# Performance work log

Hardware: AMD Instinct MI355X
Metric: run time of the kernel (lower is better)

## Reference

```python
import jax, jax.numpy as jnp
import numpy as np

K = 3          # kernel_size
STRIDE = 1
PAD = 1
DIL = 1


def setup_inputs() -> dict:
    key = jax.random.key(0)
    k1, k2, k3, k4, k5 = jax.random.split(key, 5)
    x = jax.random.normal(k1, (4, 64, 128, 128), jnp.float32)
    weight = jax.random.normal(k2, (64, 64, K, K), jnp.float32) * 0.05   # [O, C, K, K]
    bias = jax.random.normal(k3, (64,), jnp.float32) * 0.05
    # offset conv params: small nonzero so offsets actually exercise bilinear sampling
    offset_w = jax.random.normal(k4, (2 * K * K, 64, K, K), jnp.float32) * 0.01
    offset_b = jax.random.normal(k5, (2 * K * K,), jnp.float32) * 0.1
    return {"x": x, "weight": weight, "bias": bias,
            "offset_w": offset_w, "offset_b": offset_b}


def _conv2d(x, w, b):
    y = jax.lax.conv_general_dilated(
        x, w, window_strides=(STRIDE, STRIDE),
        padding=((PAD, PAD), (PAD, PAD)), rhs_dilation=(DIL, DIL),
        dimension_numbers=("NCHW", "OIHW", "NCHW"))
    return y + b[None, :, None, None]


def _bilinear_sample(img, ys, xs):
    # img: [C, H, W]; ys, xs: [KK, Ho, Wo] float sampling coords
    H, W = img.shape[1], img.shape[2]
    y0 = jnp.floor(ys)
    x0 = jnp.floor(xs)
    y1 = y0 + 1.0
    x1 = x0 + 1.0
    wy1 = ys - y0
    wx1 = xs - x0
    wy0 = 1.0 - wy1
    wx0 = 1.0 - wx1

    def gather(yy, xx):
        valid = (yy >= 0) & (yy <= H - 1) & (xx >= 0) & (xx <= W - 1)
        yi = jnp.clip(yy, 0, H - 1).astype(jnp.int32)
        xi = jnp.clip(xx, 0, W - 1).astype(jnp.int32)
        v = img[:, yi, xi]                     # [C, KK, Ho, Wo]
        return v * valid.astype(img.dtype)

    return (gather(y0, x0) * (wy0 * wx0) + gather(y0, x1) * (wy0 * wx1)
            + gather(y1, x0) * (wy1 * wx0) + gather(y1, x1) * (wy1 * wx1))


def reference(x, weight, bias, offset_w, offset_b):
    B, C, H, W = x.shape
    KK = K * K
    # offsets: [B, 2*K*K, Ho, Wo], per-location (dy, dx) for each kernel tap
    offset = _conv2d(x, offset_w, offset_b)
    Ho, Wo = offset.shape[2], offset.shape[3]
    off = offset.reshape(B, KK, 2, Ho, Wo)
    dy, dx = off[:, :, 0], off[:, :, 1]        # [B, KK, Ho, Wo]

    ki, kj = jnp.meshgrid(jnp.arange(K), jnp.arange(K), indexing="ij")
    ki = ki.reshape(KK).astype(x.dtype)
    kj = kj.reshape(KK).astype(x.dtype)
    oy = (jnp.arange(Ho) * STRIDE - PAD).astype(x.dtype)
    ox = (jnp.arange(Wo) * STRIDE - PAD).astype(x.dtype)
    base_y = oy[None, :, None] + (ki * DIL)[:, None, None]   # [KK, Ho, 1]
    base_x = ox[None, None, :] + (kj * DIL)[:, None, None]   # [KK, 1, Wo]
    ys = base_y[None] + dy                                   # [B, KK, Ho, Wo]
    xs = base_x[None] + dx

    # sampled: [B, C, KK, Ho, Wo]
    sampled = jax.vmap(_bilinear_sample)(x, ys, xs)
    w = weight.reshape(weight.shape[0], C, KK)
    out = jnp.einsum("bckhw,ock->bohw", sampled, w) + bias[None, :, None, None]
    return out
```

## Files before the change

kernel.cpp:

```cpp
#include <hip/hip_runtime.h>
#include <hip/hip_bf16.h>

#define B_ 4
#define C_ 64
#define H_ 128
#define W_ 128
#define HW_ (H_ * W_)
#define OCH_ 18

typedef __attribute__((ext_vector_type(2)))  _Float16 half2v;
typedef __attribute__((ext_vector_type(8)))  _Float16 half8;
typedef __attribute__((ext_vector_type(16))) float    f32x16;

#define W2B_ELEMS (9 * 2 * 4 * 64 * 8)
#define W2A_ELEMS (36 * 64 * 8)

#define PSTRIDE_B (6 * 128 * 16 + 16)
#define WIN_BYTES (8 * PSTRIDE_B)
#define OFFL_OFS  WIN_BYTES
#define OFFW_B    (OCH_ * 32 * 4)
#define SMEM_BYTES (WIN_BYTES + 8 * OFFW_B)

__device__ __forceinline__ unsigned short f2h(float f) {
  _Float16 h = (_Float16)f;
  return *reinterpret_cast<unsigned short*>(&h);
}
__device__ __forceinline__ half2v pkrtz(float a, float b) {
  auto p = __builtin_amdgcn_cvt_pkrtz(a, b);
  return *reinterpret_cast<half2v*>(&p);
}
__device__ __forceinline__ int swz256(int x) { return (x & 7) * 32 + (x >> 3); }
__device__ __forceinline__ int SWU(int row, int col) {
  return (((row << 7) + (col & ~3) + ((col & 3) ^ ((col >> 3) & 3))) << 4);
}

__global__ __launch_bounds__(256) void pack_w_only(
    const float* __restrict__ wmain, const float* __restrict__ offw,
    unsigned short* __restrict__ ws_u) {
  int idx = blockIdx.x * 256 + threadIdx.x;
  if (idx < W2B_ELEMS) {
    int i = idx & 7, lane = (idx >> 3) & 63, s = (idx >> 9) & 3;
    int mq = (idx >> 11) & 1, t = idx >> 12;
    int o = mq * 32 + (lane & 31);
    int c = 16 * s + (lane >> 5) * 8 + i;
    ws_u[idx] = f2h(wmain[(o * 64 + c) * 9 + t]);
  } else if (idx < W2B_ELEMS + W2A_ELEMS) {
    int j = idx - W2B_ELEMS;
    int i = j & 7, lane = (j >> 3) & 63, s = j >> 9;
    int kg = 16 * s + (lane >> 5) * 8 + i;
    int t = kg >> 6, c = kg & 63, oc = lane & 31;
    ws_u[idx] = (oc < OCH_) ? f2h(offw[(oc * 64 + c) * 9 + t]) : (unsigned short)0;
  }
}

template<int T>
__device__ __forceinline__ void tap_fast(
    const float* __restrict__ offl, int pxl, int ho, int ho0, int px,
    int lane, int laneh, const char* __restrict__ smem,
    const unsigned short* __restrict__ w2b,
    f32x16& acc0, f32x16& acc1, unsigned& fm) {
  constexpr int KI = T / 3, KJ = T - 3 * (T / 3);
  const float dy = offl[(2 * T) * 32 + pxl];
  const float dx = offl[(2 * T + 1) * 32 + pxl];
  const float ys = (float)(ho - 1 + KI) + dy;
  const float xs = (float)(px - 1 + KJ) + dx;
  const float y0f = floorf(ys), x0f = floorf(xs);
  const int y0 = (int)y0f, x0 = (int)x0f;
  const int y1 = y0 + 1, x1 = x0 + 1;
  const float wy1 = ys - y0f, wx1 = xs - x0f;
  const float wy0 = 1.f - wy1, wx0 = 1.f - wx1;
  const bool vy0 = (unsigned)y0 < (unsigned)H_, vy1 = (unsigned)y1 < (unsigned)H_;
  const bool vx0 = (unsigned)x0 < (unsigned)W_, vx1 = (unsigned)x1 < (unsigned)W_;
  const float g00 = (vy0 && vx0) ? wy0 * wx0 : 0.f;
  const float g01 = (vy0 && vx1) ? wy0 * wx1 : 0.f;
  const float g10 = (vy1 && vx0) ? wy1 * wx0 : 0.f;
  const float g11 = (vy1 && vx1) ? wy1 * wx1 : 0.f;
  const int yc0 = min(max(y0, 0), H_ - 1), yc1 = min(max(y1, 0), H_ - 1);
  const int xc0 = min(max(x0, 0), W_ - 1), xc1 = min(max(x1, 0), W_ - 1);
  const int rr0 = yc0 - ho0 + 2, rr1 = yc1 - ho0 + 2;
  const bool wr0 = (unsigned)rr0 < 6u, wr1 = (unsigned)rr1 < 6u;
  const float gg00 = wr0 ? g00 : 0.f, gg01 = wr0 ? g01 : 0.f;
  const float gg10 = wr1 ? g10 : 0.f, gg11 = wr1 ? g11 : 0.f;
  if (__any((!wr0 & (vy0 & (vx0 | vx1))) | (!wr1 & (vy1 & (vx0 | vx1)))))
    fm |= (1u << T);
  const int cr0 = min(max(rr0, 0), 5), cr1 = min(max(rr1, 0), 5);
  const int u00 = SWU(cr0, xc0), u01 = SWU(cr0, xc1);
  const int u10 = SWU(cr1, xc0), u11 = SWU(cr1, xc1);
  half2v G00; G00.x = G00.y = (_Float16)gg00;
  half2v G01; G01.x = G01.y = (_Float16)gg01;
  half2v G10; G10.x = G10.y = (_Float16)gg10;
  half2v G11; G11.x = G11.y = (_Float16)gg11;
  const unsigned short* wt2 = w2b + T * 4096;

  #pragma unroll
  for (int ss = 0; ss < 4; ++ss) {
    const char* pb = smem + (2 * ss + laneh) * PSTRIDE_B;
    const half8 c00 = *(const half8*)(pb + u00);
    const half8 c01 = *(const half8*)(pb + u01);
    const half8 c10 = *(const half8*)(pb + u10);
    const half8 c11 = *(const half8*)(pb + u11);
    const half2v* p00 = (const half2v*)&c00;
    const half2v* p01 = (const half2v*)&c01;
    const half2v* p10 = (const half2v*)&c10;
    const half2v* p11 = (const half2v*)&c11;
    union { half8 v; half2v h[4]; } bf;
    #pragma unroll
    for (int d = 0; d < 4; ++d)
      bf.h[d] = p00[d] * G00 + p01[d] * G01 + p10[d] * G10 + p11[d] * G11;
    const half8 a0 = *(const half8*)&wt2[(ss * 64 + lane) * 8];
    const half8 a1 = *(const half8*)&wt2[((4 + ss) * 64 + lane) * 8];
    acc0 = __builtin_amdgcn_mfma_f32_32x32x16_f16(a0, bf.v, acc0, 0, 0, 0);
    acc1 = __builtin_amdgcn_mfma_f32_32x32x16_f16(a1, bf.v, acc1, 0, 0, 0);
  }
}

__global__ __launch_bounds__(512, 2) void deform_fused9(
    const float* __restrict__ x, const float* __restrict__ bias,
    const float* __restrict__ ob, const unsigned short* __restrict__ w2b,
    const unsigned short* __restrict__ w2a, float* __restrict__ out) {
  const int blk = swz256(blockIdx.x);
  const int ho0 = (blk & 63) * 2;
  const int b   = blk >> 6;
  const int tid = threadIdx.x;
  const int lane = tid & 63;
  const int wave = tid >> 6;
  const int r_off = wave >> 2;
  const int pair  = wave & 3;
  const int ho = ho0 + r_off;
  const int pxl = lane & 31;
  const int px = pair * 32 + pxl;
  const int laneh = lane >> 5;

  __shared__ __align__(16) char smem[SMEM_BYTES];

  const float* xb = x + (size_t)b * C_ * HW_;
  #pragma unroll
  for (int it = 0; it < 3; ++it) {
    const int u = tid + it * 512;
    const int row  = u >> 8;
    const int p    = (u >> 5) & 7;
    const int col4 = u & 31;
    const int srow = min(H_ - 1, max(0, ho0 - 2 + row));
    const float* bp = xb + (size_t)(p * 8) * HW_ + srow * W_ + col4 * 4;
    float4 f[8];
    #pragma unroll
    for (int i = 0; i < 8; ++i) f[i] = *(const float4*)(bp + (size_t)i * HW_);
    char* outb = smem + p * PSTRIDE_B;
    #pragma unroll
    for (int j = 0; j < 4; ++j) {
      union { half8 v; half2v h[4]; } o;
      #pragma unroll
      for (int k = 0; k < 4; ++k)
        o.h[k] = pkrtz(reinterpret_cast<const float*>(&f[2 * k])[j],
                       reinterpret_cast<const float*>(&f[2 * k + 1])[j]);
      *(half8*)(outb + SWU(row, col4 * 4 + j)) = o.v;
    }
  }
  __syncthreads();

  f32x16 pacc_a, pacc_b;
  #pragma unroll
  for (int r = 0; r < 16; ++r) { pacc_a[r] = 0.f; pacc_b[r] = 0.f; }

  #pragma unroll 1
  for (int sq = 0; sq < 18; ++sq) {
    #pragma unroll
    for (int h = 0; h < 2; ++h) {
      const int s = 2 * sq + h;
      const int t = s >> 2;
      const int ki = (t >= 6) ? 2 : ((t >= 3) ? 1 : 0);
      const int kj = t - 3 * ki;
      const int row = ho - 1 + ki;
      const int col = px - 1 + kj;
      half8 bfr = {0, 0, 0, 0, 0, 0, 0, 0};
      if (((unsigned)row < (unsigned)H_) && ((unsigned)col < (unsigned)W_))
        bfr = *(const half8*)(smem + ((s & 3) * 2 + laneh) * PSTRIDE_B
                              + SWU(ki + 1 + r_off, col));
      const half8 afr = *(const half8*)&w2a[((size_t)s * 64 + lane) * 8];
      if (h)
        pacc_b = __builtin_amdgcn_mfma_f32_32x32x16_f16(afr, bfr, pacc_b, 0, 0, 0);
      else
        pacc_a = __builtin_amdgcn_mfma_f32_32x32x16_f16(afr, bfr, pacc_a, 0, 0, 0);
    }
  }

  float* offl = (float*)(smem + OFFL_OFS + wave * OFFW_B);
  #pragma unroll
  for (int reg = 0; reg < 16; ++reg) {
    const int oc = (reg & 3) + 8 * (reg >> 2) + 4 * laneh;
    if (oc < OCH_) offl[oc * 32 + pxl] = pacc_a[reg] + pacc_b[reg] + ob[oc];
  }

  f32x16 acc0, acc1;
  #pragma unroll
  for (int r = 0; r < 16; ++r) { acc0[r] = 0.f; acc1[r] = 0.f; }
  unsigned fm = 0;

  tap_fast<0>(offl, pxl, ho, ho0, px, lane, laneh, smem, w2b, acc0, acc1, fm);
  tap_fast<1>(offl, pxl, ho, ho0, px, lane, laneh, smem, w2b, acc0, acc1, fm);
  tap_fast<2>(offl, pxl, ho, ho0, px, lane, laneh, smem, w2b, acc0, acc1, fm);
  tap_fast<3>(offl, pxl, ho, ho0, px, lane, laneh, smem, w2b, acc0, acc1, fm);
  tap_fast<4>(offl, pxl, ho, ho0, px, lane, laneh, smem, w2b, acc0, acc1, fm);
  tap_fast<5>(offl, pxl, ho, ho0, px, lane, laneh, smem, w2b, acc0, acc1, fm);
  tap_fast<6>(offl, pxl, ho, ho0, px, lane, laneh, smem, w2b, acc0, acc1, fm);
  tap_fast<7>(offl, pxl, ho, ho0, px, lane, laneh, smem, w2b, acc0, acc1, fm);
  tap_fast<8>(offl, pxl, ho, ho0, px, lane, laneh, smem, w2b, acc0, acc1, fm);

  if (__builtin_expect(fm != 0, 0)) {
    #pragma unroll 1
    for (int t = 0; t < 9; ++t) {
      if (!((fm >> t) & 1)) continue;
      const int ki = (t >= 6) ? 2 : ((t >= 3) ? 1 : 0);
      const int kj = t - 3 * ki;
      const float dy = offl[(2 * t) * 32 + pxl];
      const float dx = offl[(2 * t + 1) * 32 + pxl];
      const float ys = (float)(ho - 1 + ki) + dy;
      const float xs = (float)(px - 1 + kj) + dx;
      const float y0f = floorf(ys), x0f = floorf(xs);
      const int y0 = (int)y0f, x0 = (int)x0f;
      const int y1 = y0 + 1, x1 = x0 + 1;
      const float wy1 = ys - y0f, wx1 = xs - x0f;
      const float wy0 = 1.f - wy1, wx0 = 1.f - wx1;
      const bool vy0 = (unsigned)y0 < (unsigned)H_, vy1 = (unsigned)y1 < (unsigned)H_;
      const bool vx0 = (unsigned)x0 < (unsigned)W_, vx1 = (unsigned)x1 < (unsigned)W_;
      float g00 = (vy0 && vx0) ? wy0 * wx0 : 0.f;
      float g01 = (vy0 && vx1) ? wy0 * wx1 : 0.f;
      float g10 = (vy1 && vx0) ? wy1 * wx0 : 0.f;
      float g11 = (vy1 && vx1) ? wy1 * wx1 : 0.f;
      const int yc0 = min(max(y0, 0), H_ - 1), yc1 = min(max(y1, 0), H_ - 1);
      const int xc0 = min(max(x0, 0), W_ - 1), xc1 = min(max(x1, 0), W_ - 1);
      const bool wr0 = (unsigned)(yc0 - ho0 + 2) < 6u;
      const bool wr1 = (unsigned)(yc1 - ho0 + 2) < 6u;
      g00 = wr0 ? 0.f : g00; g01 = wr0 ? 0.f : g01;
      g10 = wr1 ? 0.f : g10; g11 = wr1 ? 0.f : g11;
      const unsigned short* wt2 = w2b + t * 4096;
      #pragma unroll 1
      for (int ss = 0; ss < 4; ++ss) {
        union { half8 v; _Float16 e[8]; } bf;
        #pragma unroll
        for (int i = 0; i < 8; ++i) {
          const float* img = xb + (size_t)((2 * ss + laneh) * 8 + i) * HW_;
          float v = g00 * img[yc0 * W_ + xc0] + g01 * img[yc0 * W_ + xc1]
                  + g10 * img[yc1 * W_ + xc0] + g11 * img[yc1 * W_ + xc1];
          bf.e[i] = (_Float16)v;
        }
        const half8 a0 = *(const half8*)&wt2[(ss * 64 + lane) * 8];
        const half8 a1 = *(const half8*)&wt2[((4 + ss) * 64 + lane) * 8];
        acc0 = __builtin_amdgcn_mfma_f32_32x32x16_f16(a0, bf.v, acc0, 0, 0, 0);
        acc1 = __builtin_amdgcn_mfma_f32_32x32x16_f16(a1, bf.v, acc1, 0, 0, 0);
      }
    }
  }

  #pragma unroll
  for (int reg = 0; reg < 16; ++reg) {
    const int row = (reg & 3) + 8 * (reg >> 2) + 4 * laneh;
    out[((b * 64 + row)      * H_ + ho) * W_ + px] = acc0[reg] + bias[row];
    out[((b * 64 + 32 + row) * H_ + ho) * W_ + px] = acc1[reg] + bias[32 + row];
  }
}

extern "C" void kernel_launch(void* const* d_in, const int* in_sizes, int n_in,
                              void* d_out, int out_size, void* d_ws, size_t ws_size,
                              hipStream_t stream) {
  const float* x    = (const float*)d_in[0];
  const float* wt   = (const float*)d_in[1];
  const float* bias = (const float*)d_in[2];
  const float* ow   = (const float*)d_in[3];
  const float* ob   = (const float*)d_in[4];
  float* out = (float*)d_out;

  unsigned short* ws_u = (unsigned short*)d_ws;
  unsigned short* w2b  = ws_u;
  unsigned short* w2a  = ws_u + W2B_ELEMS;

  const int pack_blocks = (W2B_ELEMS + W2A_ELEMS + 255) / 256;
  pack_w_only<<<pack_blocks, 256, 0, stream>>>(wt, ow, ws_u);

  deform_fused9<<<B_ * (H_ / 2), 512, 0, stream>>>(x, bias, ob, w2b, w2a, out);
}
```

Before: 36.90 us.

## Split deform taps across wave groups per row with LDS reduction

Each block now handles a single output row instead of two. The two groups of four waves split the nine deformable taps between them (4 and 5) and combine partial accumulators through an LDS reduction. Offsets are pulled straight from the offset-conv MFMA registers with shuffles, so they no longer make a round trip through LDS. The smaller LDS window raises the launch-bounds occupancy hint, and the out-of-window fallback becomes a per-tap wave-uniform branch. The price is twice as many blocks, each loading its own 5-row halo, so input loads and the offset conv are duplicated, and there is an extra barrier plus reduction traffic.

```diff
diff --git a/kernel.cpp b/kernel.cpp
--- a/kernel.cpp
+++ b/kernel.cpp
@@ -15,11 +15,9 @@
 #define W2B_ELEMS (9 * 2 * 4 * 64 * 8)
 #define W2A_ELEMS (36 * 64 * 8)
 
-#define PSTRIDE_B (6 * 128 * 16 + 16)
+#define PSTRIDE_B (5 * 128 * 16)
 #define WIN_BYTES (8 * PSTRIDE_B)
-#define OFFL_OFS  WIN_BYTES
-#define OFFW_B    (OCH_ * 32 * 4)
-#define SMEM_BYTES (WIN_BYTES + 8 * OFFW_B)
+#define SMEM_BYTES WIN_BYTES
 
 __device__ __forceinline__ unsigned short f2h(float f) {
   _Float16 h = (_Float16)f;
@@ -29,7 +27,7 @@
   auto p = __builtin_amdgcn_cvt_pkrtz(a, b);
   return *reinterpret_cast<half2v*>(&p);
 }
-__device__ __forceinline__ int swz256(int x) { return (x & 7) * 32 + (x >> 3); }
+__device__ __forceinline__ int swz512(int x) { return (x & 7) * 64 + (x >> 3); }
 __device__ __forceinline__ int SWU(int row, int col) {
   return (((row << 7) + (col & ~3) + ((col & 3) ^ ((col >> 3) & 3))) << 4);
 }
@@ -54,14 +52,12 @@
 }
 
 template<int T>
-__device__ __forceinline__ void tap_fast(
-    const float* __restrict__ offl, int pxl, int ho, int ho0, int px,
-    int lane, int laneh, const char* __restrict__ smem,
+__device__ __forceinline__ void tap_full(
+    float dy, float dx, int ho, int px, int lane, int laneh,
+    const char* __restrict__ smem, const float* __restrict__ xb,
     const unsigned short* __restrict__ w2b,
-    f32x16& acc0, f32x16& acc1, unsigned& fm) {
+    f32x16& acc0, f32x16& acc1) {
   constexpr int KI = T / 3, KJ = T - 3 * (T / 3);
-  const float dy = offl[(2 * T) * 32 + pxl];
-  const float dx = offl[(2 * T + 1) * 32 + pxl];
   const float ys = (float)(ho - 1 + KI) + dy;
   const float xs = (float)(px - 1 + KJ) + dx;
   const float y0f = floorf(ys), x0f = floorf(xs);
@@ -77,32 +73,52 @@
   const float g11 = (vy1 && vx1) ? wy1 * wx1 : 0.f;
   const int yc0 = min(max(y0, 0), H_ - 1), yc1 = min(max(y1, 0), H_ - 1);
   const int xc0 = min(max(x0, 0), W_ - 1), xc1 = min(max(x1, 0), W_ - 1);
-  const int rr0 = yc0 - ho0 + 2, rr1 = yc1 - ho0 + 2;
-  const bool wr0 = (unsigned)rr0 < 6u, wr1 = (unsigned)rr1 < 6u;
-  const float gg00 = wr0 ? g00 : 0.f, gg01 = wr0 ? g01 : 0.f;
-  const float gg10 = wr1 ? g10 : 0.f, gg11 = wr1 ? g11 : 0.f;
-  if (__any((!wr0 & (vy0 & (vx0 | vx1))) | (!wr1 & (vy1 & (vx0 | vx1)))))
-    fm |= (1u << T);
-  const int cr0 = min(max(rr0, 0), 5), cr1 = min(max(rr1, 0), 5);
+  const int rr0 = yc0 - ho + 2, rr1 = yc1 - ho + 2;
+  const bool in = ((unsigned)rr0 < 5u) & ((unsigned)rr1 < 5u);
+  const unsigned short* wt2 = w2b + T * 4096;
+
+  if (__builtin_expect(__any(!in), 0)) {
+    #pragma unroll 1
+    for (int ss = 0; ss < 4; ++ss) {
+      union { half8 v; _Float16 e[8]; } bf;
+      #pragma unroll
+      for (int i = 0; i < 8; ++i) {
+        const float* img = xb + (size_t)((2 * ss + laneh) * 8 + i) * HW_;
+        float v = g00 * img[yc0 * W_ + xc0] + g01 * img[yc0 * W_ + xc1]
+                + g10 * img[yc1 * W_ + xc0] + g11 * img[yc1 * W_ + xc1];
+        bf.e[i] = (_Float16)v;
+      }
+      const half8 a0 = *(const half8*)&wt2[(ss * 64 + lane) * 8];
+      const half8 a1 = *(const half8*)&wt2[((4 + ss) * 64 + lane) * 8];
+      acc0 = __builtin_amdgcn_mfma_f32_32x32x16_f16(a0, bf.v, acc0, 0, 0, 0);
+      acc1 = __builtin_amdgcn_mfma_f32_32x32x16_f16(a1, bf.v, acc1, 0, 0, 0);
+    }
+    return;
+  }
+
+  const int cr0 = min(max(rr0, 0), 4), cr1 = min(max(rr1, 0), 4);
   const int u00 = SWU(cr0, xc0), u01 = SWU(cr0, xc1);
   const int u10 = SWU(cr1, xc0), u11 = SWU(cr1, xc1);
-  half2v G00; G00.x = G00.y = (_Float16)gg00;
-  half2v G01; G01.x = G01.y = (_Float16)gg01;
-  half2v G10; G10.x = G10.y = (_Float16)gg10;
-  half2v G11; G11.x = G11.y = (_Float16)gg11;
-  const unsigned short* wt2 = w2b + T * 4096;
-
+  half2v G00; G00.x = G00.y = (_Float16)g00;
+  half2v G01; G01.x = G01.y = (_Float16)g01;
+  half2v G10; G10.x = G10.y = (_Float16)g10;
+  half2v G11; G11.x = G11.y = (_Float16)g11;
+
+  half8 c00[4], c01[4], c10[4], c11[4];
   #pragma unroll
   for (int ss = 0; ss < 4; ++ss) {
     const char* pb = smem + (2 * ss + laneh) * PSTRIDE_B;
-    const half8 c00 = *(const half8*)(pb + u00);
-    const half8 c01 = *(const half8*)(pb + u01);
-    const half8 c10 = *(const half8*)(pb + u10);
-    const half8 c11 = *(const half8*)(pb + u11);
-    const half2v* p00 = (const half2v*)&c00;
-    const half2v* p01 = (const half2v*)&c01;
-    const half2v* p10 = (const half2v*)&c10;
-    const half2v* p11 = (const half2v*)&c11;
+    c00[ss] = *(const half8*)(pb + u00);
+    c01[ss] = *(const half8*)(pb + u01);
+    c10[ss] = *(const half8*)(pb + u10);
+    c11[ss] = *(const half8*)(pb + u11);
+  }
+  #pragma unroll
+  for (int ss = 0; ss < 4; ++ss) {
+    const half2v* p00 = (const half2v*)&c00[ss];
+    const half2v* p01 = (const half2v*)&c01[ss];
+    const half2v* p10 = (const half2v*)&c10[ss];
+    const half2v* p11 = (const half2v*)&c11[ss];
     union { half8 v; half2v h[4]; } bf;
     #pragma unroll
     for (int d = 0; d < 4; ++d)
@@ -114,19 +130,27 @@
   }
 }
 
-__global__ __launch_bounds__(512, 2) void deform_fused9(
+#define EXT(T, DY, DX)                                                                  \
+  {                                                                                     \
+    constexpr int ocy = 2 * (T), ocx = 2 * (T) + 1;                                     \
+    constexpr int ry = (ocy & 3) + 4 * (ocy >> 3), hy = (ocy >> 2) & 1;                 \
+    constexpr int rx = (ocx & 3) + 4 * (ocx >> 3), hx = (ocx >> 2) & 1;                 \
+    DY = __shfl(pacc[ry], (lane & 31) + (hy << 5)) + ob[ocy];                           \
+    DX = __shfl(pacc[rx], (lane & 31) + (hx << 5)) + ob[ocx];                           \
+  }
+
+__global__ __launch_bounds__(512, 4) void deform_fused10(
     const float* __restrict__ x, const float* __restrict__ bias,
     const float* __restrict__ ob, const unsigned short* __restrict__ w2b,
     const unsigned short* __restrict__ w2a, float* __restrict__ out) {
-  const int blk = swz256(blockIdx.x);
-  const int ho0 = (blk & 63) * 2;
-  const int b   = blk >> 6;
+  const int blk = swz512(blockIdx.x);
+  const int ho = blk & (H_ - 1);
+  const int b  = blk >> 7;
   const int tid = threadIdx.x;
   const int lane = tid & 63;
   const int wave = tid >> 6;
-  const int r_off = wave >> 2;
-  const int pair  = wave & 3;
-  const int ho = ho0 + r_off;
+  const int pair = wave & 3;
+  const int sub  = wave >> 2;
   const int pxl = lane & 31;
   const int px = pair * 32 + pxl;
   const int laneh = lane >> 5;
@@ -137,23 +161,25 @@
   #pragma unroll
   for (int it = 0; it < 3; ++it) {
     const int u = tid + it * 512;
-    const int row  = u >> 8;
-    const int p    = (u >> 5) & 7;
-    const int col4 = u & 31;
-    const int srow = min(H_ - 1, max(0, ho0 - 2 + row));
-    const float* bp = xb + (size_t)(p * 8) * HW_ + srow * W_ + col4 * 4;
-    float4 f[8];
-    #pragma unroll
-    for (int i = 0; i < 8; ++i) f[i] = *(const float4*)(bp + (size_t)i * HW_);
-    char* outb = smem + p * PSTRIDE_B;
-    #pragma unroll
-    for (int j = 0; j < 4; ++j) {
-      union { half8 v; half2v h[4]; } o;
+    if (u < 1280) {
+      const int row  = u >> 8;
+      const int p    = (u >> 5) & 7;
+      const int col4 = u & 31;
+      const int srow = min(H_ - 1, max(0, ho - 2 + row));
+      const float* bp = xb + (size_t)(p * 8) * HW_ + srow * W_ + col4 * 4;
+      float4 f[8];
       #pragma unroll
-      for (int k = 0; k < 4; ++k)
-        o.h[k] = pkrtz(reinterpret_cast<const float*>(&f[2 * k])[j],
-                       reinterpret_cast<const float*>(&f[2 * k + 1])[j]);
-      *(half8*)(outb + SWU(row, col4 * 4 + j)) = o.v;
+      for (int i = 0; i < 8; ++i) f[i] = *(const float4*)(bp + (size_t)i * HW_);
+      char* outb = smem + p * PSTRIDE_B;
+      #pragma unroll
+      for (int j = 0; j < 4; ++j) {
+        union { half8 v; half2v h[4]; } o;
+        #pragma unroll
+        for (int k = 0; k < 4; ++k)
+          o.h[k] = pkrtz(reinterpret_cast<const float*>(&f[2 * k])[j],
+                         reinterpret_cast<const float*>(&f[2 * k + 1])[j]);
+        *(half8*)(outb + SWU(row, col4 * 4 + j)) = o.v;
+      }
     }
   }
   __syncthreads();
@@ -175,7 +201,7 @@
       half8 bfr = {0, 0, 0, 0, 0, 0, 0, 0};
       if (((unsigned)row < (unsigned)H_) && ((unsigned)col < (unsigned)W_))
         bfr = *(const half8*)(smem + ((s & 3) * 2 + laneh) * PSTRIDE_B
-                              + SWU(ki + 1 + r_off, col));
+                              + SWU(ki + 1, col));
       const half8 afr = *(const half8*)&w2a[((size_t)s * 64 + lane) * 8];
       if (h)
         pacc_b = __builtin_amdgcn_mfma_f32_32x32x16_f16(afr, bfr, pacc_b, 0, 0, 0);
@@ -183,80 +209,54 @@
         pacc_a = __builtin_amdgcn_mfma_f32_32x32x16_f16(afr, bfr, pacc_a, 0, 0, 0);
     }
   }
-
-  float* offl = (float*)(smem + OFFL_OFS + wave * OFFW_B);
-  #pragma unroll
-  for (int reg = 0; reg < 16; ++reg) {
-    const int oc = (reg & 3) + 8 * (reg >> 2) + 4 * laneh;
-    if (oc < OCH_) offl[oc * 32 + pxl] = pacc_a[reg] + pacc_b[reg] + ob[oc];
-  }
+  f32x16 pacc;
+  #pragma unroll
+  for (int r = 0; r < 16; ++r) pacc[r] = pacc_a[r] + pacc_b[r];
 
   f32x16 acc0, acc1;
   #pragma unroll
   for (int r = 0; r < 16; ++r) { acc0[r] = 0.f; acc1[r] = 0.f; }
-  unsigned fm = 0;
-
-  tap_fast<0>(offl, pxl, ho, ho0, px, lane, laneh, smem, w2b, acc0, acc1, fm);
-  tap_fast<1>(offl, pxl, ho, ho0, px, lane, laneh, smem, w2b, acc0, acc1, fm);
-  tap_fast<2>(offl, pxl, ho, ho0, px, lane, laneh, smem, w2b, acc0, acc1, fm);
-  tap_fast<3>(offl, pxl, ho, ho0, px, lane, laneh, smem, w2b, acc0, acc1, fm);
-  tap_fast<4>(offl, pxl, ho, ho0, px, lane, laneh, smem, w2b, acc0, acc1, fm);
-  tap_fast<5>(offl, pxl, ho, ho0, px, lane, laneh, smem, w2b, acc0, acc1, fm);
-  tap_fast<6>(offl, pxl, ho, ho0, px, lane, laneh, smem, w2b, acc0, acc1, fm);
-  tap_fast<7>(offl, pxl, ho, ho0, px, lane, laneh, smem, w2b, acc0, acc1, fm);
-  tap_fast<8>(offl, pxl, ho, ho0, px, lane, laneh, smem, w2b, acc0, acc1, fm);
-
-  if (__builtin_expect(fm != 0, 0)) {
-    #pragma unroll 1
-    for (int t = 0; t < 9; ++t) {
-      if (!((fm >> t) & 1)) continue;
-      const int ki = (t >= 6) ? 2 : ((t >= 3) ? 1 : 0);
-      const int kj = t - 3 * ki;
-      const float dy = offl[(2 * t) * 32 + pxl];
-      const float dx = offl[(2 * t + 1) * 32 + pxl];
-      const float ys = (float)(ho - 1 + ki) + dy;
-      const float xs = (float)(px - 1 + kj) + dx;
-      const float y0f = floorf(ys), x0f = floorf(xs);
-      const int y0 = (int)y0f, x0 = (int)x0f;
-      const int y1 = y0 + 1, x1 = x0 + 1;
-      const float wy1 = ys - y0f, wx1 = xs - x0f;
-      const float wy0 = 1.f - wy1, wx0 = 1.f - wx1;
-      const bool vy0 = (unsigned)y0 < (unsigned)H_, vy1 = (unsigned)y1 < (unsigned)H_;
-      const bool vx0 = (unsigned)x0 < (unsigned)W_, vx1 = (unsigned)x1 < (unsigned)W_;
-      float g00 = (vy0 && vx0) ? wy0 * wx0 : 0.f;
-      float g01 = (vy0 && vx1) ? wy0 * wx1 : 0.f;
-      float g10 = (vy1 && vx0) ? wy1 * wx0 : 0.f;
-      float g11 = (vy1 && vx1) ? wy1 * wx1 : 0.f;
-      const int yc0 = min(max(y0, 0), H_ - 1), yc1 = min(max(y1, 0), H_ - 1);
-      const int xc0 = min(max(x0, 0), W_ - 1), xc1 = min(max(x1, 0), W_ - 1);
-      const bool wr0 = (unsigned)(yc0 - ho0 + 2) < 6u;
-      const bool wr1 = (unsigned)(yc1 - ho0 + 2) < 6u;
-      g00 = wr0 ? 0.f : g00; g01 = wr0 ? 0.f : g01;
-      g10 = wr1 ? 0.f : g10; g11 = wr1 ? 0.f : g11;
-      const unsigned short* wt2 = w2b + t * 4096;
-      #pragma unroll 1
-      for (int ss = 0; ss < 4; ++ss) {
-        union { half8 v; _Float16 e[8]; } bf;
-        #pragma unroll
-        for (int i = 0; i < 8; ++i) {
-          const float* img = xb + (size_t)((2 * ss + laneh) * 8 + i) * HW_;
-          float v = g00 * img[yc0 * W_ + xc0] + g01 * img[yc0 * W_ + xc1]
-                  + g10 * img[yc1 * W_ + xc0] + g11 * img[yc1 * W_ + xc1];
-          bf.e[i] = (_Float16)v;
-        }
-        const half8 a0 = *(const half8*)&wt2[(ss * 64 + lane) * 8];
-        const half8 a1 = *(const half8*)&wt2[((4 + ss) * 64 + lane) * 8];
-        acc0 = __builtin_amdgcn_mfma_f32_32x32x16_f16(a0, bf.v, acc0, 0, 0, 0);
-        acc1 = __builtin_amdgcn_mfma_f32_32x32x16_f16(a1, bf.v, acc1, 0, 0, 0);
-      }
-    }
-  }
-
-  #pragma unroll
-  for (int reg = 0; reg < 16; ++reg) {
-    const int row = (reg & 3) + 8 * (reg >> 2) + 4 * laneh;
-    out[((b * 64 + row)      * H_ + ho) * W_ + px] = acc0[reg] + bias[row];
-    out[((b * 64 + 32 + row) * H_ + ho) * W_ + px] = acc1[reg] + bias[32 + row];
+
+  if (sub == 0) {
+    float d0y, d0x, d1y, d1x, d2y, d2x, d3y, d3x;
+    EXT(0, d0y, d0x); EXT(1, d1y, d1x); EXT(2, d2y, d2x); EXT(3, d3y, d3x);
+    tap_full<0>(d0y, d0x, ho, px, lane, laneh, smem, xb, w2b, acc0, acc1);
+    tap_full<1>(d1y, d1x, ho, px, lane, laneh, smem, xb, w2b, acc0, acc1);
+    tap_full<2>(d2y, d2x, ho, px, lane, laneh, smem, xb, w2b, acc0, acc1);
+    tap_full<3>(d3y, d3x, ho, px, lane, laneh, smem, xb, w2b, acc0, acc1);
+  } else {
+    float d4y, d4x, d5y, d5x, d6y, d6x, d7y, d7x, d8y, d8x;
+    EXT(4, d4y, d4x); EXT(5, d5y, d5x); EXT(6, d6y, d6x);
+    EXT(7, d7y, d7x); EXT(8, d8y, d8x);
+    tap_full<4>(d4y, d4x, ho, px, lane, laneh, smem, xb, w2b, acc0, acc1);
+    tap_full<5>(d5y, d5x, ho, px, lane, laneh, smem, xb, w2b, acc0, acc1);
+    tap_full<6>(d6y, d6x, ho, px, lane, laneh, smem, xb, w2b, acc0, acc1);
+    tap_full<7>(d7y, d7x, ho, px, lane, laneh, smem, xb, w2b, acc0, acc1);
+    tap_full<8>(d8y, d8x, ho, px, lane, laneh, smem, xb, w2b, acc0, acc1);
+  }
+
+  __syncthreads();
+  float* red = (float*)smem;
+  if (sub) {
+    #pragma unroll
+    for (int i = 0; i < 16; ++i) {
+      red[(i * 4 + pair) * 64 + lane]        = acc0[i];
+      red[((16 + i) * 4 + pair) * 64 + lane] = acc1[i];
+    }
+  }
+  __syncthreads();
+  if (!sub) {
+    #pragma unroll
+    for (int i = 0; i < 16; ++i) {
+      acc0[i] += red[(i * 4 + pair) * 64 + lane];
+      acc1[i] += red[((16 + i) * 4 + pair) * 64 + lane];
+    }
+    #pragma unroll
+    for (int reg = 0; reg < 16; ++reg) {
+      const int row = (reg & 3) + 8 * (reg >> 2) + 4 * laneh;
+      out[((b * 64 + row)      * H_ + ho) * W_ + px] = acc0[reg] + bias[row];
+      out[((b * 64 + 32 + row) * H_ + ho) * W_ + px] = acc1[reg] + bias[32 + row];
+    }
   }
 }
 
@@ -277,5 +277,5 @@
   const int pack_blocks = (W2B_ELEMS + W2A_ELEMS + 255) / 256;
   pack_w_only<<<pack_blocks, 256, 0, stream>>>(wt, ow, ws_u);
 
-  deform_fused9<<<B_ * (H_ / 2), 512, 0, stream>>>(x, bias, ob, w2b, w2a, out);
-}
+  deform_fused10<<<B_ * H_, 512, 0, stream>>>(x, bias, ob, w2b, w2a, out);
+}
```

New measurement: 38.76 us. 5.0% more time.
